# Performance work log

Measured on AMD Instinct MI355X. Metric: run time of the kernel, lower is better.

Reference implementation:

```python
import jax, jax.numpy as jnp
import numpy as np

WS, SHIFT, HEADS, DIM = 64, 32, 8, 256
BIN_X, BIN_Y, BIN_Z = 51, 51, 11
GRID = 111.32 / 100.0  # degree2km / 100


def setup_inputs() -> dict:
    key = jax.random.key(0)
    ks = jax.random.split(key, 10)
    B, H, W, C = 2, 512, 16, DIM
    x = jax.random.normal(ks[0], (B, H, W, C), jnp.float32)
    loc = jax.random.normal(ks[1], (B, W, 3), jnp.float32) * 5.0  # station xyz (km-ish)
    qkv_weight = jax.random.normal(ks[2], (3 * C, C), jnp.float32) * (C ** -0.5)
    qkv_bias = jax.random.normal(ks[3], (3 * C,), jnp.float32) * 0.02
    proj_weight = jax.random.normal(ks[4], (C, C), jnp.float32) * (C ** -0.5)
    proj_bias = jax.random.normal(ks[5], (C,), jnp.float32) * 0.02
    table_t = jax.random.normal(ks[6], (2 * WS - 1, HEADS), jnp.float32) * 0.1
    table_x = jax.random.normal(ks[7], (BIN_X, HEADS), jnp.float32) * 0.1
    table_y = jax.random.normal(ks[8], (BIN_Y, HEADS), jnp.float32) * 0.1
    table_z = jax.random.normal(ks[9], (BIN_Z, HEADS), jnp.float32) * 0.1
    return dict(x=x, loc=loc, qkv_weight=qkv_weight, qkv_bias=qkv_bias,
                proj_weight=proj_weight, proj_bias=proj_bias,
                table_t=table_t, table_x=table_x, table_y=table_y, table_z=table_z)


def _rel_bias(loc, table_t, table_x, table_y, table_z):
    # Faithful to the torch code, including its .repeat tiling patterns:
    #   time term indexes with (i % WS, j % WS); station terms with (i % W, j % W).
    B, W, _ = loc.shape
    t = jnp.arange(WS)
    rel_t = jnp.tile(t[:, None] - t[None, :] + (WS - 1), (W, W))  # [N, N]
    rel = loc[:, :, None, :] - loc[:, None, :, :]                 # [B, W, W, 3]

    def bin_idx(v, nbins):
        return jnp.clip(jnp.round(v / GRID + (nbins - 1) / 2.0), 0, nbins - 1).astype(jnp.int32)

    ix = jnp.tile(bin_idx(rel[..., 0], BIN_X), (1, WS, WS))  # [B, N, N]
    iy = jnp.tile(bin_idx(rel[..., 1], BIN_Y), (1, WS, WS))
    iz = jnp.tile(bin_idx(rel[..., 2], BIN_Z), (1, WS, WS))
    bias = table_t[rel_t][None] + table_x[ix] + table_y[iy] + table_z[iz]  # [B, N, N, heads]
    return bias.transpose(0, 3, 1, 2)  # [B, heads, N, N]


def reference(x, loc, qkv_weight, qkv_bias, proj_weight, proj_bias,
              table_t, table_x, table_y, table_z):
    B, H, W, C = x.shape
    hd = C // HEADS
    pad_b = (-H) % WS
    xp = jnp.pad(x, ((0, 0), (0, pad_b), (0, 0), (0, 0)))
    pad_H = H + pad_b
    shift = 0 if WS >= pad_H else SHIFT  # static python decision, matches torch
    if shift > 0:
        xp = jnp.roll(xp, -shift, axis=1)
    nW = pad_H // WS
    N = WS * W
    # view/permute of a size-1 axis is a no-op on layout -> plain reshape
    xw = xp.reshape(B * nW, N, C)

    qkv = xw @ qkv_weight.T + qkv_bias                     # [B*nW, N, 3C]
    qkv = qkv.reshape(B * nW, N, 3, HEADS, hd).transpose(2, 0, 3, 1, 4)
    q, k, v = qkv[0] * (hd ** -0.5), qkv[1], qkv[2]        # [B*nW, heads, N, hd]
    attn = jnp.einsum('whqd,whkd->whqk', q, k)             # [B*nW, heads, N, N]

    bias = _rel_bias(loc, table_t, table_x, table_y, table_z)  # [B, heads, N, N]
    attn = attn.reshape(B, nW, HEADS, N, N) + bias[:, None]

    if shift > 0:
        # torch w_slices degenerate to the full-width slice, so the region label
        # depends only on the (rolled) time index: 2 / 5 / 8.
        h = jnp.arange(pad_H)
        row = jnp.where(h < pad_H - WS, 2.0, jnp.where(h < pad_H - shift, 5.0, 8.0))
        m = jnp.broadcast_to(row.reshape(nW, WS, 1), (nW, WS, W)).reshape(nW, N)
        diff = m[:, :, None] - m[:, None, :]               # [nW, N, N]
        attn = attn + jnp.where(diff != 0.0, -100.0, 0.0)[None, :, None]

    attn = jax.nn.softmax(attn.reshape(B * nW, HEADS, N, N), axis=-1)
    out = jnp.einsum('whqk,whkd->wqhd', attn, v).reshape(B * nW, N, C)
    out = out @ proj_weight.T + proj_bias
    out = out.reshape(B, pad_H, W, C)
    if shift > 0:
        out = jnp.roll(out, shift, axis=1)
    return out[:, :H]
```

## Files before the change

kernel.cpp:

```cpp
#include <hip/hip_runtime.h>
#include <hip/hip_bf16.h>

typedef __bf16 bf16;
typedef __bf16 bf16x8 __attribute__((ext_vector_type(8)));
typedef float f32x4 __attribute__((ext_vector_type(4)));
typedef unsigned short u16;

static constexpr size_t OFF_Q    = 0;
static constexpr size_t OFF_K    = 8388608;
static constexpr size_t OFF_VT   = 16777216;
static constexpr size_t OFF_Y    = 25165824;
static constexpr size_t OFF_COMB = 33554432;
static constexpr size_t OFF_PWB  = 33816576;
static constexpr size_t OFF_WB   = 33947648;
static constexpr size_t OFF_BMAX = 34340864;
static constexpr size_t OFF_GM   = 34340928;

static constexpr float LOG2E = 1.4426950408889634f;

__device__ __forceinline__ int clampi(int v, int lo, int hi) {
  return v < lo ? lo : (v > hi ? hi : v);
}

__device__ __forceinline__ void glds16(const bf16* src, bf16* dst) {
  __builtin_amdgcn_global_load_lds((const __attribute__((address_space(1))) void*)src,
                                   (__attribute__((address_space(3))) void*)dst,
                                   16, 0, 0);
}

__device__ __forceinline__ bf16x8 cvt8(const float* p) {
  f32x4 a = *(const f32x4*)p;
  f32x4 b = *(const f32x4*)(p + 4);
  bf16x8 r;
  r[0] = (bf16)a[0]; r[1] = (bf16)a[1]; r[2] = (bf16)a[2]; r[3] = (bf16)a[3];
  r[4] = (bf16)b[0]; r[5] = (bf16)b[1]; r[6] = (bf16)b[2]; r[7] = (bf16)b[3];
  return r;
}

__global__ void build_comb_k(const float* __restrict__ loc, const float* __restrict__ tt,
                             const float* __restrict__ tx, const float* __restrict__ ty,
                             const float* __restrict__ tz, float* __restrict__ comb,
                             float* __restrict__ bmax) {
  const int b = blockIdx.x >> 3, h = blockIdx.x & 7;
  __shared__ float st[256];
  __shared__ float red[256];
  const int t = threadIdx.x;
  {
    const int i = t >> 4, j = t & 15;
    const float* li = loc + (b * 16 + i) * 3;
    const float* lj = loc + (b * 16 + j) * 3;
    const float G = (float)(111.32 / 100.0);
    float dx = li[0] - lj[0];
    float dy = li[1] - lj[1];
    float dz = li[2] - lj[2];
    int ix = clampi((int)rintf(dx / G + 25.0f), 0, 50);
    int iy = clampi((int)rintf(dy / G + 25.0f), 0, 50);
    int iz = clampi((int)rintf(dz / G + 5.0f), 0, 10);
    st[t] = tx[ix * 8 + h] + ty[iy * 8 + h] + tz[iz * 8 + h];
  }
  __syncthreads();
  float* out = comb + blockIdx.x * 4096;
  float lm = -1e30f;
  for (int e = t; e < 4096; e += 256) {
    int a = e >> 6, c = e & 63;
    float v = tt[(a - c + 63) * 8 + h] + st[((a & 15) << 4) | (c & 15)];
    out[e] = v;
    lm = fmaxf(lm, v);
  }
  red[t] = lm;
  __syncthreads();
  for (int s = 128; s > 0; s >>= 1) {
    if (t < s) red[t] = fmaxf(red[t], red[t + s]);
    __syncthreads();
  }
  if (t == 0) bmax[blockIdx.x] = red[0];
}

__global__ __launch_bounds__(256) void cvt_all_k(const float* __restrict__ x, const float* __restrict__ w,
                                                 const float* __restrict__ pw, bf16* __restrict__ xb,
                                                 bf16* __restrict__ wb, bf16* __restrict__ pwb) {
  const int bid = blockIdx.x;
  if (bid < 2048) {
    const int tid = bid * 256 + threadIdx.x;
    const int e = tid * 8;
    const int m = e >> 8, k = e & 255;
    const int wid = m >> 10, n = m & 1023;
    const int bb = wid >> 3, wi = wid & 7, tw = n >> 4, ww = n & 15;
    const int hh = (wi * 64 + tw + 32) & 511;
    const float* src = x + (((bb * 512 + hh) * 16 + ww) << 8) + k;
    *(bf16x8*)(xb + e) = cvt8(src);
  } else {
    const int tid = (bid - 2048) * 256 + threadIdx.x;
    const int e = tid * 8;
    if (e < 768 * 256) {
      *(bf16x8*)(wb + e) = cvt8(w + e);
    } else {
      const int e2 = e - 768 * 256;
      *(bf16x8*)(pwb + e2) = cvt8(pw + e2);
    }
  }
}

__global__ __launch_bounds__(256) void qkv_k(const bf16* __restrict__ xb, const bf16* __restrict__ wb,
                                             const float* __restrict__ qb, bf16* __restrict__ qws,
                                             bf16* __restrict__ kws, bf16* __restrict__ vtws) {
  __shared__ __align__(16) bf16 lA[128 * 64];
  __shared__ __align__(16) bf16 lB[128 * 64];
  const int lane = threadIdx.x & 63, wv = threadIdx.x >> 6;
  const int rr = lane & 15, g = lane >> 4;
  const int wr = wv >> 1, wc = wv & 1;
  const int bid = blockIdx.x;
  const int tt = (bid & 7) * 96 + (bid >> 3);
  const int mtile = tt / 6, ntile = tt % 6;
  const int mb = mtile * 128, nb2 = ntile * 128;
  const int arow = lane >> 3;
  const int sg = ((lane & 7) ^ arow) << 3;
  const int axor = rr & 7;
  f32x4 acc[4][4] = {};
  for (int kb = 0; kb < 256; kb += 64) {
#pragma unroll
    for (int q = 0; q < 4; ++q) {
      const int rowp = (wv * 4 + q) * 8 + arow;
      glds16(xb + (mb + rowp) * 256 + kb + sg, &lA[(wv * 4 + q) * 512]);
      glds16(wb + (nb2 + rowp) * 256 + kb + sg, &lB[(wv * 4 + q) * 512]);
    }
    __syncthreads();
#pragma unroll
    for (int ks = 0; ks < 2; ++ks) {
      bf16x8 af[4], bfr[4];
#pragma unroll
      for (int rt = 0; rt < 4; ++rt)
        af[rt] = *(const bf16x8*)&lA[(wr * 64 + rt * 16 + rr) * 64 + (((ks << 2) | g) ^ axor) * 8];
#pragma unroll
      for (int ct = 0; ct < 4; ++ct)
        bfr[ct] = *(const bf16x8*)&lB[(wc * 64 + ct * 16 + rr) * 64 + (((ks << 2) | g) ^ axor) * 8];
#pragma unroll
      for (int rt = 0; rt < 4; ++rt)
#pragma unroll
        for (int ct = 0; ct < 4; ++ct)
          acc[rt][ct] = __builtin_amdgcn_mfma_f32_16x16x32_bf16(af[rt], bfr[ct], acc[rt][ct], 0, 0, 0);
    }
    __syncthreads();
  }
  const int qkvi = (nb2 >> 8);
  const float mult = (qkvi == 0) ? 0.17677669529663687f * 1.4426950408889634f : 1.0f;
#pragma unroll
  for (int ct = 0; ct < 4; ++ct) {
    const int c2 = nb2 + wc * 64 + ct * 16 + rr;
    const float bc = qb[c2];
    const int h2 = (c2 & 255) >> 5, d = c2 & 31;
#pragma unroll
    for (int rt = 0; rt < 4; ++rt) {
      const int m0 = mb + wr * 64 + rt * 16 + g * 4;
      const int wid = m0 >> 10, n0 = m0 & 1023;
      if (qkvi == 2) {
        union { u16 us[4]; uint2 u2; } pk;
#pragma unroll
        for (int r = 0; r < 4; ++r) {
          bf16 bv = (bf16)(acc[rt][ct][r] + bc);
          pk.us[r] = *(const u16*)&bv;
        }
        *(uint2*)(vtws + ((size_t)((wid * 8 + h2) * 32 + d) << 10) + n0) = pk.u2;
      } else {
        bf16* bp = (qkvi ? kws : qws) + ((size_t)(wid * 8 + h2) << 15) + d;
#pragma unroll
        for (int r = 0; r < 4; ++r) bp[(size_t)(n0 + r) << 5] = (bf16)((acc[rt][ct][r] + bc) * mult);
      }
    }
  }
}

__global__ __launch_bounds__(256) void norm_k(const bf16* __restrict__ qws, const bf16* __restrict__ kws,
                                              const float* __restrict__ bmax, float* __restrict__ gM) {
  const int grp = blockIdx.x;
  const int t = threadIdx.x;
  const bf16* qb = qws + ((size_t)grp << 15);
  const bf16* kb = kws + ((size_t)grp << 15);
  float qm = 0.0f, km = 0.0f;
#pragma unroll
  for (int rw = 0; rw < 4; ++rw) {
    const int r = rw * 256 + t;
    float sq = 0.0f, sk = 0.0f;
#pragma unroll
    for (int d8 = 0; d8 < 4; ++d8) {
      bf16x8 vq = *(const bf16x8*)(qb + r * 32 + d8 * 8);
      bf16x8 vk = *(const bf16x8*)(kb + r * 32 + d8 * 8);
#pragma unroll
      for (int e = 0; e < 8; ++e) {
        float a = (float)vq[e]; sq += a * a;
        float c = (float)vk[e]; sk += c * c;
      }
    }
    qm = fmaxf(qm, sq); km = fmaxf(km, sk);
  }
  __shared__ float rq[256], rk[256];
  rq[t] = qm; rk[t] = km;
  __syncthreads();
  for (int s = 128; s > 0; s >>= 1) {
    if (t < s) { rq[t] = fmaxf(rq[t], rq[t + s]); rk[t] = fmaxf(rk[t], rk[t + s]); }
    __syncthreads();
  }
  if (t == 0) {
    const int b = grp >> 6, h = grp & 7;
    gM[grp] = sqrtf(rq[0] * rk[0]) * 1.0005f + bmax[b * 8 + h] * LOG2E + 0.01f;
  }
}

__global__ __launch_bounds__(256, 4)
void attn_k(const bf16* __restrict__ qws, const bf16* __restrict__ kws,
            const bf16* __restrict__ vtws, const float* __restrict__ comb,
            const float* __restrict__ gM, bf16* __restrict__ yws) {
  const int lane = threadIdx.x & 63, wv = threadIdx.x >> 6;
  const int rr = lane & 15, g = lane >> 4;
  const int id = blockIdx.x;
  const int xcd = id & 7, t2 = id >> 3;
  const int qt = t2 & 7, gh = t2 >> 3;
  const int grp = gh * 8 + xcd;
  const int h = grp & 7, wid = grp >> 3;
  const int b = wid >> 3;
  const bool win7 = (wid & 7) == 7;
  const int iA = qt * 128 + wv * 16 + rr;
  const int iB = iA + 64;
  const bf16* qbase = qws + ((size_t)grp << 15);
  const bf16* kbase = kws + ((size_t)grp << 15);
  const bf16* vbase = vtws + ((size_t)grp << 15);
  const bf16x8 qfA = *(const bf16x8*)(qbase + (iA << 5) + g * 8);
  const bf16x8 qfB = *(const bf16x8*)(qbase + (iB << 5) + g * 8);
  const float* crow = comb + (b * 8 + h) * 4096 + (iA & 63) * 64;
  f32x4 b00 = *(const f32x4*)(crow + g * 8);
  f32x4 b01 = *(const f32x4*)(crow + g * 8 + 4);
  f32x4 b10 = *(const f32x4*)(crow + 32 + g * 8);
  f32x4 b11 = *(const f32x4*)(crow + 32 + g * 8 + 4);
  const bool ilow = iA < 512;
  const float M = gM[grp];
  const float MASKL = -100.0f * LOG2E;
  const float cLo = ((win7 && !ilow) ? MASKL : 0.0f) - M;
  const float cHi = ((win7 && ilow) ? MASKL : 0.0f) - M;
#pragma unroll
  for (int r = 0; r < 4; ++r) {
    b00[r] = b00[r] * LOG2E + cLo; b01[r] = b01[r] * LOG2E + cLo;
    b10[r] = b10[r] * LOG2E + cLo; b11[r] = b11[r] * LOG2E + cLo;
  }

  const int kp = 8 * (rr >> 2) + (rr & 3);
  const bf16* krow = kbase + (kp << 5) + g * 8;
  const bf16* vrow0 = vbase + (rr << 10) + g * 8;
  const bf16* vrow1 = vbase + ((16 + rr) << 10) + g * 8;

  f32x4 o0A = {}, o1A = {}, o0B = {}, o1B = {};
  f32x4 laA = {}, laB = {};

#define ATTN_STEP32(KB, B0, B1)                                                        \
  {                                                                                    \
    const int kb_ = (KB);                                                              \
    bf16x8 kA = *(const bf16x8*)(krow + (kb_ << 5));                                   \
    bf16x8 kB = *(const bf16x8*)(krow + ((kb_ + 4) << 5));                             \
    bf16x8 vA = *(const bf16x8*)(vrow0 + kb_);                                         \
    bf16x8 vB = *(const bf16x8*)(vrow1 + kb_);                                         \
    f32x4 zero = {};                                                                   \
    f32x4 sA0 = __builtin_amdgcn_mfma_f32_16x16x32_bf16(kA, qfA, zero, 0, 0, 0);       \
    f32x4 sA1 = __builtin_amdgcn_mfma_f32_16x16x32_bf16(kB, qfA, zero, 0, 0, 0);       \
    f32x4 sB0 = __builtin_amdgcn_mfma_f32_16x16x32_bf16(kA, qfB, zero, 0, 0, 0);       \
    f32x4 sB1 = __builtin_amdgcn_mfma_f32_16x16x32_bf16(kB, qfB, zero, 0, 0, 0);       \
    f32x4 pA0, pA1, pB0, pB1;                                                          \
    _Pragma("unroll")                                                                  \
    for (int r = 0; r < 4; ++r) {                                                      \
      pA0[r] = __builtin_amdgcn_exp2f(sA0[r] + B0[r]);                                 \
      pA1[r] = __builtin_amdgcn_exp2f(sA1[r] + B1[r]);                                 \
      pB0[r] = __builtin_amdgcn_exp2f(sB0[r] + B0[r]);                                 \
      pB1[r] = __builtin_amdgcn_exp2f(sB1[r] + B1[r]);                                 \
    }                                                                                  \
    laA += pA0 + pA1; laB += pB0 + pB1;                                                \
    bf16x8 paA, paB;                                                                   \
    _Pragma("unroll")                                                                  \
    for (int r = 0; r < 4; ++r) {                                                      \
      paA[r] = (bf16)pA0[r]; paA[r + 4] = (bf16)pA1[r];                                \
      paB[r] = (bf16)pB0[r]; paB[r + 4] = (bf16)pB1[r];                                \
    }                                                                                  \
    o0A = __builtin_amdgcn_mfma_f32_16x16x32_bf16(vA, paA, o0A, 0, 0, 0);              \
    o1A = __builtin_amdgcn_mfma_f32_16x16x32_bf16(vB, paA, o1A, 0, 0, 0);              \
    o0B = __builtin_amdgcn_mfma_f32_16x16x32_bf16(vA, paB, o0B, 0, 0, 0);              \
    o1B = __builtin_amdgcn_mfma_f32_16x16x32_bf16(vB, paB, o1B, 0, 0, 0);              \
  }

#pragma unroll
  for (int t = 0; t < 8; ++t) {
    ATTN_STEP32(t * 64, b00, b01);
    ATTN_STEP32(t * 64 + 32, b10, b11);
  }
  {
    const float dlt = cHi - cLo;
#pragma unroll
    for (int r = 0; r < 4; ++r) { b00[r] += dlt; b01[r] += dlt; b10[r] += dlt; b11[r] += dlt; }
  }
#pragma unroll
  for (int t = 8; t < 16; ++t) {
    ATTN_STEP32(t * 64, b00, b01);
    ATTN_STEP32(t * 64 + 32, b10, b11);
  }
#undef ATTN_STEP32

  {
    float l = (laA[0] + laA[1]) + (laA[2] + laA[3]);
    l += __shfl_xor(l, 16);
    l += __shfl_xor(l, 32);
    const float inv = 1.0f / l;
    bf16* ybase = yws + (size_t)((wid << 10) + iA) * 256 + h * 32;
    union { u16 us[4]; uint2 u2; } pk;
#pragma unroll
    for (int r = 0; r < 4; ++r) { bf16 bv = (bf16)(o0A[r] * inv); pk.us[r] = *(const u16*)&bv; }
    *(uint2*)(ybase + g * 4) = pk.u2;
#pragma unroll
    for (int r = 0; r < 4; ++r) { bf16 bv = (bf16)(o1A[r] * inv); pk.us[r] = *(const u16*)&bv; }
    *(uint2*)(ybase + 16 + g * 4) = pk.u2;
  }
  {
    float l = (laB[0] + laB[1]) + (laB[2] + laB[3]);
    l += __shfl_xor(l, 16);
    l += __shfl_xor(l, 32);
    const float inv = 1.0f / l;
    bf16* ybase = yws + (size_t)((wid << 10) + iB) * 256 + h * 32;
    union { u16 us[4]; uint2 u2; } pk;
#pragma unroll
    for (int r = 0; r < 4; ++r) { bf16 bv = (bf16)(o0B[r] * inv); pk.us[r] = *(const u16*)&bv; }
    *(uint2*)(ybase + g * 4) = pk.u2;
#pragma unroll
    for (int r = 0; r < 4; ++r) { bf16 bv = (bf16)(o1B[r] * inv); pk.us[r] = *(const u16*)&bv; }
    *(uint2*)(ybase + 16 + g * 4) = pk.u2;
  }
}

__global__ __launch_bounds__(256) void proj_k(const bf16* __restrict__ yws, const bf16* __restrict__ pwb,
                                              const float* __restrict__ pb, float* __restrict__ out) {
  __shared__ __align__(16) bf16 lA[128 * 64];
  __shared__ __align__(16) bf16 lB[128 * 64];
  const int lane = threadIdx.x & 63, wv = threadIdx.x >> 6;
  const int rr = lane & 15, g = lane >> 4;
  const int wr = wv >> 1, wc = wv & 1;
  const int bid = blockIdx.x;
  const int tt = (bid & 7) * 32 + (bid >> 3);
  const int mtile = tt >> 1, ntile = tt & 1;
  const int mb = mtile * 128, nb2 = ntile * 128;
  const int arow = lane >> 3;
  const int sg = ((lane & 7) ^ arow) << 3;
  const int axor = rr & 7;
  f32x4 acc[4][4] = {};
  for (int kb = 0; kb < 256; kb += 64) {
#pragma unroll
    for (int q = 0; q < 4; ++q) {
      const int rowp = (wv * 4 + q) * 8 + arow;
      glds16(yws + (size_t)(mb + rowp) * 256 + kb + sg, &lA[(wv * 4 + q) * 512]);
      glds16(pwb + (nb2 + rowp) * 256 + kb + sg, &lB[(wv * 4 + q) * 512]);
    }
    __syncthreads();
#pragma unroll
    for (int ks = 0; ks < 2; ++ks) {
      bf16x8 af[4], bfr[4];
#pragma unroll
      for (int rt = 0; rt < 4; ++rt)
        af[rt] = *(const bf16x8*)&lA[(wr * 64 + rt * 16 + rr) * 64 + (((ks << 2) | g) ^ axor) * 8];
#pragma unroll
      for (int ct = 0; ct < 4; ++ct)
        bfr[ct] = *(const bf16x8*)&lB[(wc * 64 + ct * 16 + rr) * 64 + (((ks << 2) | g) ^ axor) * 8];
#pragma unroll
      for (int rt = 0; rt < 4; ++rt)
#pragma unroll
        for (int ct = 0; ct < 4; ++ct)
          acc[rt][ct] = __builtin_amdgcn_mfma_f32_16x16x32_bf16(af[rt], bfr[ct], acc[rt][ct], 0, 0, 0);
    }
    __syncthreads();
  }
#pragma unroll
  for (int ct = 0; ct < 4; ++ct) {
    const int c2 = nb2 + wc * 64 + ct * 16 + rr;
    const float bc = pb[c2];
#pragma unroll
    for (int rt = 0; rt < 4; ++rt) {
#pragma unroll
      for (int r = 0; r < 4; ++r) {
        const int m = mb + wr * 64 + rt * 16 + g * 4 + r;
        const int wid = m >> 10, n = m & 1023;
        const int bb = wid >> 3;
        const int hh = ((wid & 7) * 64 + (n >> 4) + 32) & 511;
        out[(((bb * 512 + hh) * 16 + (n & 15)) << 8) + c2] = acc[rt][ct][r] + bc;
      }
    }
  }
}

extern "C" void kernel_launch(void* const* d_in, const int* in_sizes, int n_in,
                              void* d_out, int out_size, void* d_ws, size_t ws_size,
                              hipStream_t stream) {
  const float* x     = (const float*)d_in[0];
  const float* loc   = (const float*)d_in[1];
  const float* qkvw  = (const float*)d_in[2];
  const float* qkvb  = (const float*)d_in[3];
  const float* projw = (const float*)d_in[4];
  const float* projb = (const float*)d_in[5];
  const float* tt    = (const float*)d_in[6];
  const float* tx    = (const float*)d_in[7];
  const float* ty    = (const float*)d_in[8];
  const float* tz    = (const float*)d_in[9];
  char* ws = (char*)d_ws;
  bf16* qws   = (bf16*)(ws + OFF_Q);
  bf16* kws   = (bf16*)(ws + OFF_K);
  bf16* vtws  = (bf16*)(ws + OFF_VT);
  bf16* yws   = (bf16*)(ws + OFF_Y);
  bf16* xb    = (bf16*)(ws + OFF_Y);
  float* comb = (float*)(ws + OFF_COMB);
  bf16* pwb   = (bf16*)(ws + OFF_PWB);
  bf16* wb    = (bf16*)(ws + OFF_WB);
  float* bmax = (float*)(ws + OFF_BMAX);
  float* gM   = (float*)(ws + OFF_GM);
  float* out = (float*)d_out;

  build_comb_k<<<16, 256, 0, stream>>>(loc, tt, tx, ty, tz, comb, bmax);
  cvt_all_k<<<2176, 256, 0, stream>>>(x, qkvw, projw, xb, wb, pwb);
  qkv_k<<<768, 256, 0, stream>>>(xb, wb, qkvb, qws, kws, vtws);
  norm_k<<<128, 256, 0, stream>>>(qws, kws, bmax, gM);
  attn_k<<<1024, 256, 0, stream>>>(qws, kws, vtws, comb, gM, yws);
  proj_k<<<256, 256, 0, stream>>>(yws, pwb, projb, out);
}
```

Measured before the change: 95.88 us.

## Split attention key range across two blocks and combine partial outputs

Splits each attention block's key range into two halves processed by separate blocks, doubling the grid to 2048 blocks. Each half writes fp32 partial outputs and row sums, using the output buffer and extra workspace as scratch, and a new combine kernel sums and normalizes them into bf16. This works because a fixed global max is used instead of an online softmax. The aim is more parallelism and occupancy on the attention stage, at the cost of an extra kernel launch and roughly 32 MB of extra fp32 traffic. It falls back to the monolithic kernel when the workspace is too small.

```diff
diff --git a/kernel.cpp b/kernel.cpp
--- a/kernel.cpp
+++ b/kernel.cpp
@@ -15,6 +15,9 @@
 static constexpr size_t OFF_WB   = 33947648;
 static constexpr size_t OFF_BMAX = 34340864;
 static constexpr size_t OFF_GM   = 34340928;
+static constexpr size_t OFF_OP1  = 34603008;
+static constexpr size_t OFF_LA   = 51380224;
+static constexpr size_t WS_NEED  = 52428800;
 
 static constexpr float LOG2E = 1.4426950408889634f;
 
@@ -206,48 +209,32 @@
   }
 }
 
-__global__ __launch_bounds__(256, 4)
-void attn_k(const bf16* __restrict__ qws, const bf16* __restrict__ kws,
-            const bf16* __restrict__ vtws, const float* __restrict__ comb,
-            const float* __restrict__ gM, bf16* __restrict__ yws) {
-  const int lane = threadIdx.x & 63, wv = threadIdx.x >> 6;
-  const int rr = lane & 15, g = lane >> 4;
-  const int id = blockIdx.x;
-  const int xcd = id & 7, t2 = id >> 3;
-  const int qt = t2 & 7, gh = t2 >> 3;
-  const int grp = gh * 8 + xcd;
-  const int h = grp & 7, wid = grp >> 3;
-  const int b = wid >> 3;
-  const bool win7 = (wid & 7) == 7;
-  const int iA = qt * 128 + wv * 16 + rr;
-  const int iB = iA + 64;
-  const bf16* qbase = qws + ((size_t)grp << 15);
-  const bf16* kbase = kws + ((size_t)grp << 15);
-  const bf16* vbase = vtws + ((size_t)grp << 15);
-  const bf16x8 qfA = *(const bf16x8*)(qbase + (iA << 5) + g * 8);
-  const bf16x8 qfB = *(const bf16x8*)(qbase + (iB << 5) + g * 8);
-  const float* crow = comb + (b * 8 + h) * 4096 + (iA & 63) * 64;
-  f32x4 b00 = *(const f32x4*)(crow + g * 8);
-  f32x4 b01 = *(const f32x4*)(crow + g * 8 + 4);
-  f32x4 b10 = *(const f32x4*)(crow + 32 + g * 8);
-  f32x4 b11 = *(const f32x4*)(crow + 32 + g * 8 + 4);
-  const bool ilow = iA < 512;
-  const float M = gM[grp];
-  const float MASKL = -100.0f * LOG2E;
-  const float cLo = ((win7 && !ilow) ? MASKL : 0.0f) - M;
-  const float cHi = ((win7 && ilow) ? MASKL : 0.0f) - M;
-#pragma unroll
-  for (int r = 0; r < 4; ++r) {
-    b00[r] = b00[r] * LOG2E + cLo; b01[r] = b01[r] * LOG2E + cLo;
-    b10[r] = b10[r] * LOG2E + cLo; b11[r] = b11[r] * LOG2E + cLo;
-  }
-
-  const int kp = 8 * (rr >> 2) + (rr & 3);
-  const bf16* krow = kbase + (kp << 5) + g * 8;
-  const bf16* vrow0 = vbase + (rr << 10) + g * 8;
-  const bf16* vrow1 = vbase + ((16 + rr) << 10) + g * 8;
-
-  f32x4 o0A = {}, o1A = {}, o0B = {}, o1B = {};
+#define ATTN_PROLOG                                                                     \
+  const int lane = threadIdx.x & 63, wv = threadIdx.x >> 6;                             \
+  const int rr = lane & 15, g = lane >> 4;                                              \
+  const bf16* qbase = qws + ((size_t)grp << 15);                                        \
+  const bf16* kbase = kws + ((size_t)grp << 15);                                        \
+  const bf16* vbase = vtws + ((size_t)grp << 15);                                       \
+  const int h = grp & 7, wid = grp >> 3;                                                \
+  const int b = wid >> 3;                                                               \
+  const bool win7 = (wid & 7) == 7;                                                     \
+  const int iA = qt * 128 + wv * 16 + rr;                                               \
+  const int iB = iA + 64;                                                               \
+  const bf16x8 qfA = *(const bf16x8*)(qbase + (iA << 5) + g * 8);                       \
+  const bf16x8 qfB = *(const bf16x8*)(qbase + (iB << 5) + g * 8);                       \
+  const float* crow = comb + (b * 8 + h) * 4096 + (iA & 63) * 64;                       \
+  f32x4 b00 = *(const f32x4*)(crow + g * 8);                                            \
+  f32x4 b01 = *(const f32x4*)(crow + g * 8 + 4);                                        \
+  f32x4 b10 = *(const f32x4*)(crow + 32 + g * 8);                                       \
+  f32x4 b11 = *(const f32x4*)(crow + 32 + g * 8 + 4);                                   \
+  const bool ilow = iA < 512;                                                           \
+  const float M = gM[grp];                                                              \
+  const float MASKL = -100.0f * LOG2E;                                                  \
+  const int kp = 8 * (rr >> 2) + (rr & 3);                                              \
+  const bf16* krow = kbase + (kp << 5) + g * 8;                                         \
+  const bf16* vrow0 = vbase + (rr << 10) + g * 8;                                       \
+  const bf16* vrow1 = vbase + ((16 + rr) << 10) + g * 8;                                \
+  f32x4 o0A = {}, o1A = {}, o0B = {}, o1B = {};                                         \
   f32x4 laA = {}, laB = {};
 
 #define ATTN_STEP32(KB, B0, B1)                                                        \
@@ -283,6 +270,22 @@
     o1B = __builtin_amdgcn_mfma_f32_16x16x32_bf16(vB, paB, o1B, 0, 0, 0);              \
   }
 
+__global__ __launch_bounds__(256, 4)
+void attn_mono_k(const bf16* __restrict__ qws, const bf16* __restrict__ kws,
+                 const bf16* __restrict__ vtws, const float* __restrict__ comb,
+                 const float* __restrict__ gM, bf16* __restrict__ yws) {
+  const int id = blockIdx.x;
+  const int xcd = id & 7, t2 = id >> 3;
+  const int qt = t2 & 7, gh = t2 >> 3;
+  const int grp = gh * 8 + xcd;
+  ATTN_PROLOG
+  const float cLo = ((win7 && !ilow) ? MASKL : 0.0f) - M;
+  const float cHi = ((win7 && ilow) ? MASKL : 0.0f) - M;
+#pragma unroll
+  for (int r = 0; r < 4; ++r) {
+    b00[r] = b00[r] * LOG2E + cLo; b01[r] = b01[r] * LOG2E + cLo;
+    b10[r] = b10[r] * LOG2E + cLo; b11[r] = b11[r] * LOG2E + cLo;
+  }
 #pragma unroll
   for (int t = 0; t < 8; ++t) {
     ATTN_STEP32(t * 64, b00, b01);
@@ -298,8 +301,6 @@
     ATTN_STEP32(t * 64, b00, b01);
     ATTN_STEP32(t * 64 + 32, b10, b11);
   }
-#undef ATTN_STEP32
-
   {
     float l = (laA[0] + laA[1]) + (laA[2] + laA[3]);
     l += __shfl_xor(l, 16);
@@ -328,6 +329,72 @@
     for (int r = 0; r < 4; ++r) { bf16 bv = (bf16)(o1B[r] * inv); pk.us[r] = *(const u16*)&bv; }
     *(uint2*)(ybase + 16 + g * 4) = pk.u2;
   }
+}
+
+__global__ __launch_bounds__(256, 4)
+void attn_split_k(const bf16* __restrict__ qws, const bf16* __restrict__ kws,
+                  const bf16* __restrict__ vtws, const float* __restrict__ comb,
+                  const float* __restrict__ gM, float* __restrict__ oP0,
+                  float* __restrict__ oP1, float* __restrict__ laP) {
+  const int id = blockIdx.x;
+  const int xcd = id & 7, t2 = id >> 3;
+  const int half = t2 & 1, qt = (t2 >> 1) & 7, gh = t2 >> 4;
+  const int grp = gh * 8 + xcd;
+  ATTN_PROLOG
+  const bool maskme = win7 && (half ? ilow : !ilow);
+  const float cM = (maskme ? MASKL : 0.0f) - M;
+#pragma unroll
+  for (int r = 0; r < 4; ++r) {
+    b00[r] = b00[r] * LOG2E + cM; b01[r] = b01[r] * LOG2E + cM;
+    b10[r] = b10[r] * LOG2E + cM; b11[r] = b11[r] * LOG2E + cM;
+  }
+  const int kb0 = half << 9;
+#pragma unroll
+  for (int t = 0; t < 8; ++t) {
+    ATTN_STEP32(kb0 + t * 64, b00, b01);
+    ATTN_STEP32(kb0 + t * 64 + 32, b10, b11);
+  }
+  float* op = half ? oP1 : oP0;
+  {
+    float l = (laA[0] + laA[1]) + (laA[2] + laA[3]);
+    l += __shfl_xor(l, 16);
+    l += __shfl_xor(l, 32);
+    float* ob = op + (size_t)((wid << 10) + iA) * 256 + h * 32;
+    *(f32x4*)(ob + g * 4) = o0A;
+    *(f32x4*)(ob + 16 + g * 4) = o1A;
+    if (g == 0) laP[(half << 17) + (grp << 10) + iA] = l;
+  }
+  {
+    float l = (laB[0] + laB[1]) + (laB[2] + laB[3]);
+    l += __shfl_xor(l, 16);
+    l += __shfl_xor(l, 32);
+    float* ob = op + (size_t)((wid << 10) + iB) * 256 + h * 32;
+    *(f32x4*)(ob + g * 4) = o0B;
+    *(f32x4*)(ob + 16 + g * 4) = o1B;
+    if (g == 0) laP[(half << 17) + (grp << 10) + iB] = l;
+  }
+}
+
+__global__ __launch_bounds__(256) void combine_k(const float* __restrict__ oP0, const float* __restrict__ oP1,
+                                                 const float* __restrict__ laP, bf16* __restrict__ yws) {
+  const int tid = blockIdx.x * 256 + threadIdx.x;
+  const int e = tid * 8;
+  const int m = e >> 8, c = e & 255;
+  const int wid = m >> 10, i = m & 1023, h = c >> 5;
+  const int li = (((wid << 3) + h) << 10) + i;
+  const float l = laP[li] + laP[(1 << 17) + li];
+  const float inv = 1.0f / l;
+  f32x4 a0 = *(const f32x4*)(oP0 + e);
+  f32x4 a1 = *(const f32x4*)(oP0 + e + 4);
+  f32x4 c0 = *(const f32x4*)(oP1 + e);
+  f32x4 c1 = *(const f32x4*)(oP1 + e + 4);
+  bf16x8 r;
+#pragma unroll
+  for (int j = 0; j < 4; ++j) {
+    r[j] = (bf16)((a0[j] + c0[j]) * inv);
+    r[j + 4] = (bf16)((a1[j] + c1[j]) * inv);
+  }
+  *(bf16x8*)(yws + e) = r;
 }
 
 __global__ __launch_bounds__(256) void proj_k(const bf16* __restrict__ yws, const bf16* __restrict__ pwb,
@@ -418,6 +485,14 @@
   cvt_all_k<<<2176, 256, 0, stream>>>(x, qkvw, projw, xb, wb, pwb);
   qkv_k<<<768, 256, 0, stream>>>(xb, wb, qkvb, qws, kws, vtws);
   norm_k<<<128, 256, 0, stream>>>(qws, kws, bmax, gM);
-  attn_k<<<1024, 256, 0, stream>>>(qws, kws, vtws, comb, gM, yws);
+  if (ws_size >= WS_NEED) {
+    float* oP0 = (float*)d_out;
+    float* oP1 = (float*)(ws + OFF_OP1);
+    float* laP = (float*)(ws + OFF_LA);
+    attn_split_k<<<2048, 256, 0, stream>>>(qws, kws, vtws, comb, gM, oP0, oP1, laP);
+    combine_k<<<2048, 256, 0, stream>>>(oP0, oP1, laP, yws);
+  } else {
+    attn_mono_k<<<1024, 256, 0, stream>>>(qws, kws, vtws, comb, gM, yws);
+  }
   proj_k<<<256, 256, 0, stream>>>(yws, pwb, projb, out);
 }
```

After: 132.9 us. +38.6%, slower.
